# Optimization experiments

Measured on AMD Instinct MI355X. Metric: run time of the kernel, lower is better.

The kernel has to match this reference:

```python
import jax, jax.numpy as jnp
import numpy as np

ZERO_POINT = 128.0  # affine zero point for uint8-style storage


def setup_inputs() -> dict:
    key = jax.random.key(0)
    k1, k2, k3, k4 = jax.random.split(key, 4)
    B, S, IN, OUT = 4, 128, 4096, 11008
    inp = jax.random.normal(k1, (B, S, IN), dtype=jnp.float32)
    qweight = jax.random.randint(k2, (OUT, IN), 0, 256, dtype=jnp.int32)
    scale = jax.random.uniform(k3, (OUT, 1), dtype=jnp.float32) * 0.02 + 1e-4
    bias = jax.random.normal(k4, (OUT,), dtype=jnp.float32)
    return {"input": inp, "qweight": qweight, "scale": scale, "bias": bias}


def reference(input, qweight, scale, bias):
    # dequantize: per-out-channel affine, weight[o, i] = scale[o] * (q[o, i] - zp)
    weight = scale * (qweight.astype(jnp.float32) - ZERO_POINT)  # [OUT, IN]
    # F.linear(input, weight, bias) == input @ weight.T + bias
    return jnp.einsum("bsi,oi->bso", input, weight) + bias
```

## Files before the change

kernel.cpp:

```cpp
#include <hip/hip_runtime.h>
#include <hip/hip_bf16.h>


#define BM 64
#define BN 128
#define BK 64

typedef __attribute__((ext_vector_type(8))) short bf16x8;
typedef __attribute__((ext_vector_type(4))) float f32x4;

__device__ __forceinline__ unsigned short f2bf(float x) {
  __hip_bfloat16 h = __float2bfloat16(x);
  return *reinterpret_cast<unsigned short*>(&h);
}

__global__ __launch_bounds__(256, 3)
void qlinear_kernel(const float* __restrict__ A,
                    const int*   __restrict__ Q,
                    const float* __restrict__ scale,
                    const float* __restrict__ bias,
                    float* __restrict__ C,
                    int M, int N, int K)
{
  __shared__ unsigned short sA[2][BM][BK];
  __shared__ unsigned short sB[2][BN][BK];

  const int tid  = threadIdx.x;
  const int lane = tid & 63;
  const int wave = tid >> 6;
  const int wr   = wave >> 1;
  const int wc   = wave & 1;

  const int nbm  = M / BM;
  const int bm   = blockIdx.x % nbm;
  const int bn   = blockIdx.x / nbm;
  const int row0 = bm * BM;
  const int col0 = bn * BN;

  const int sr   = tid >> 4;
  const int scol = (tid & 15) << 2;

  const float* Abase = A + (size_t)(row0 + sr) * K + scol;
  const int*   Qbase = Q + (size_t)(col0 + sr) * K + scol;

  f32x4 acc[2][4];
#pragma unroll
  for (int i = 0; i < 2; ++i)
#pragma unroll
    for (int j = 0; j < 4; ++j)
      acc[i][j] = (f32x4)0.0f;

  float4 pa[4];
  int4   pq[8];

  auto LOADS = [&](int ke) {
#pragma unroll
    for (int it = 0; it < 4; ++it)
      pa[it] = *reinterpret_cast<const float4*>(Abase + (size_t)(it * 16) * K + ke);
#pragma unroll
    for (int it = 0; it < 8; ++it)
      pq[it] = *reinterpret_cast<const int4*>(Qbase + (size_t)(it * 16) * K + ke);
  };

  auto STORES = [&](int b) {
#pragma unroll
    for (int it = 0; it < 4; ++it) {
      const int r = it * 16 + sr;
      const int c = scol ^ ((r & 7) << 3);
      ushort4 h;
      h.x = f2bf(pa[it].x); h.y = f2bf(pa[it].y);
      h.z = f2bf(pa[it].z); h.w = f2bf(pa[it].w);
      *reinterpret_cast<ushort4*>(&sA[b][r][c]) = h;
    }
#pragma unroll
    for (int it = 0; it < 8; ++it) {
      const int r = it * 16 + sr;
      const int c = scol ^ ((r & 7) << 3);
      const int4 v = pq[it];
      ushort4 h;
      h.x = f2bf((float)(v.x - 128));
      h.y = f2bf((float)(v.y - 128));
      h.z = f2bf((float)(v.z - 128));
      h.w = f2bf((float)(v.w - 128));
      *reinterpret_cast<ushort4*>(&sB[b][r][c]) = h;
    }
  };

  const int NT = K / BK;
  LOADS(0);
  STORES(0);
  __syncthreads();

  for (int kt = 0; kt < NT; ++kt) {
    const int cur = kt & 1;
    if (kt + 1 < NT) LOADS((kt + 1) * BK);

#pragma unroll
    for (int kk = 0; kk < BK; kk += 32) {
      const int kb = kk + ((lane >> 4) << 3);
      bf16x8 af[2], bv[4];
#pragma unroll
      for (int mi = 0; mi < 2; ++mi) {
        const int r = wr * 32 + mi * 16 + (lane & 15);
        af[mi] = *reinterpret_cast<const bf16x8*>(&sA[cur][r][kb ^ ((r & 7) << 3)]);
      }
#pragma unroll
      for (int ni = 0; ni < 4; ++ni) {
        const int r = wc * 64 + ni * 16 + (lane & 15);
        bv[ni] = *reinterpret_cast<const bf16x8*>(&sB[cur][r][kb ^ ((r & 7) << 3)]);
      }
#pragma unroll
      for (int mi = 0; mi < 2; ++mi)
#pragma unroll
        for (int ni = 0; ni < 4; ++ni)
          acc[mi][ni] = __builtin_amdgcn_mfma_f32_16x16x32_bf16(af[mi], bv[ni], acc[mi][ni], 0, 0, 0);
    }

    if (kt + 1 < NT) STORES(cur ^ 1);
    __syncthreads();
  }

  const int cl = lane & 15;
  const int rb = row0 + wr * 32 + ((lane >> 4) << 2);
#pragma unroll
  for (int ni = 0; ni < 4; ++ni) {
    const int n = col0 + wc * 64 + ni * 16 + cl;
    const float s = scale[n];
    const float b = bias[n];
#pragma unroll
    for (int mi = 0; mi < 2; ++mi) {
#pragma unroll
      for (int r = 0; r < 4; ++r) {
        C[(size_t)(rb + mi * 16 + r) * N + n] = acc[mi][ni][r] * s + b;
      }
    }
  }
}

extern "C" void kernel_launch(void* const* d_in, const int* in_sizes, int n_in,
                              void* d_out, int out_size, void* d_ws, size_t ws_size,
                              hipStream_t stream) {
  const float* inp   = (const float*)d_in[0];
  const int*   qw    = (const int*)d_in[1];
  const float* scale = (const float*)d_in[2];
  const float* bias  = (const float*)d_in[3];
  float*       out   = (float*)d_out;

  const int OUT = in_sizes[3];
  const int IN  = in_sizes[1] / OUT;
  const int M   = in_sizes[0] / IN;

  const int grid = (M / BM) * (OUT / BN);
  qlinear_kernel<<<grid, 256, 0, stream>>>(inp, qw, scale, bias, out, M, OUT, IN);
}
```

Before: 396.5 us.

## Deepen global-load prefetch to two stages with XCD-aware block remapping

Adds a second register prefetch buffer so global loads for tile t+2 are issued while tile t is computed, giving loads more time in flight. It replaces __syncthreads with an LDS-only wait plus a raw barrier, and uses sched_barrier to keep the compiler from moving the loads. It also remaps block IDs across 8 groups to suit the XCD chiplets and lowers the occupancy hint from 3 to 2 blocks per CU to make room for the extra prefetch registers. The cost is higher register pressure and possibly lower occupancy.

```diff
diff --git a/kernel.cpp b/kernel.cpp
--- a/kernel.cpp
+++ b/kernel.cpp
@@ -14,7 +14,7 @@
   return *reinterpret_cast<unsigned short*>(&h);
 }
 
-__global__ __launch_bounds__(256, 3)
+__global__ __launch_bounds__(256, 2)
 void qlinear_kernel(const float* __restrict__ A,
                     const int*   __restrict__ Q,
                     const float* __restrict__ scale,
@@ -31,9 +31,14 @@
   const int wr   = wave >> 1;
   const int wc   = wave & 1;
 
-  const int nbm  = M / BM;
-  const int bm   = blockIdx.x % nbm;
-  const int bn   = blockIdx.x / nbm;
+  const int nbm = M / BM;
+  const int nwg = gridDim.x;
+  int wgid = blockIdx.x;
+  if ((nwg & 7) == 0) {
+    wgid = (wgid & 7) * (nwg >> 3) + (wgid >> 3);
+  }
+  const int bm   = wgid % nbm;
+  const int bn   = wgid / nbm;
   const int row0 = bm * BM;
   const int col0 = bn * BN;
 
@@ -50,10 +55,10 @@
     for (int j = 0; j < 4; ++j)
       acc[i][j] = (f32x4)0.0f;
 
-  float4 pa[4];
-  int4   pq[8];
+  float4 pa0[4], pa1[4];
+  int4   pq0[8], pq1[8];
 
-  auto LOADS = [&](int ke) {
+  auto LOADS = [&](float4* pa, int4* pq, int ke) {
 #pragma unroll
     for (int it = 0; it < 4; ++it)
       pa[it] = *reinterpret_cast<const float4*>(Abase + (size_t)(it * 16) * K + ke);
@@ -62,7 +67,7 @@
       pq[it] = *reinterpret_cast<const int4*>(Qbase + (size_t)(it * 16) * K + ke);
   };
 
-  auto STORES = [&](int b) {
+  auto STORES = [&](const float4* pa, const int4* pq, int b) {
 #pragma unroll
     for (int it = 0; it < 4; ++it) {
       const int r = it * 16 + sr;
@@ -86,15 +91,7 @@
     }
   };
 
-  const int NT = K / BK;
-  LOADS(0);
-  STORES(0);
-  __syncthreads();
-
-  for (int kt = 0; kt < NT; ++kt) {
-    const int cur = kt & 1;
-    if (kt + 1 < NT) LOADS((kt + 1) * BK);
-
+  auto COMPUTE = [&](int b) {
 #pragma unroll
     for (int kk = 0; kk < BK; kk += 32) {
       const int kb = kk + ((lane >> 4) << 3);
@@ -102,12 +99,12 @@
 #pragma unroll
       for (int mi = 0; mi < 2; ++mi) {
         const int r = wr * 32 + mi * 16 + (lane & 15);
-        af[mi] = *reinterpret_cast<const bf16x8*>(&sA[cur][r][kb ^ ((r & 7) << 3)]);
+        af[mi] = *reinterpret_cast<const bf16x8*>(&sA[b][r][kb ^ ((r & 7) << 3)]);
       }
 #pragma unroll
       for (int ni = 0; ni < 4; ++ni) {
         const int r = wc * 64 + ni * 16 + (lane & 15);
-        bv[ni] = *reinterpret_cast<const bf16x8*>(&sB[cur][r][kb ^ ((r & 7) << 3)]);
+        bv[ni] = *reinterpret_cast<const bf16x8*>(&sB[b][r][kb ^ ((r & 7) << 3)]);
       }
 #pragma unroll
       for (int mi = 0; mi < 2; ++mi)
@@ -115,9 +112,33 @@
         for (int ni = 0; ni < 4; ++ni)
           acc[mi][ni] = __builtin_amdgcn_mfma_f32_16x16x32_bf16(af[mi], bv[ni], acc[mi][ni], 0, 0, 0);
     }
+  };
 
-    if (kt + 1 < NT) STORES(cur ^ 1);
-    __syncthreads();
+  auto BAR = [&]() {
+    asm volatile("s_waitcnt lgkmcnt(0)" ::: "memory");
+    __builtin_amdgcn_s_barrier();
+  };
+
+  const int NT = K / BK;
+
+  LOADS(pa0, pq0, 0);
+  LOADS(pa1, pq1, BK);
+  __builtin_amdgcn_sched_barrier(0);
+  STORES(pa0, pq0, 0);
+  BAR();
+
+  for (int t = 0; t < NT; t += 2) {
+    if (t + 2 < NT) LOADS(pa0, pq0, (t + 2) * BK);
+    __builtin_amdgcn_sched_barrier(0);
+    COMPUTE(0);
+    STORES(pa1, pq1, 1);
+    BAR();
+
+    if (t + 3 < NT) LOADS(pa1, pq1, (t + 3) * BK);
+    __builtin_amdgcn_sched_barrier(0);
+    COMPUTE(1);
+    if (t + 2 < NT) STORES(pa0, pq0, 0);
+    BAR();
   }
 
   const int cl = lane & 15;
```

Measured after the change: 360.6 us. -9.1%, faster.
